# Kernel optimization log

Hardware: AMD Instinct MI355X
Metric: run time of the kernel (lower is better)

Reference implementation:

```python
import jax, jax.numpy as jnp
import numpy as np

OUT_F = 8192
IN_F = 8192
RANK = 32
N_TOK = 128


def _pack_ternary(w_q):
    """Pack int8 ternary {-1,0,+1} [out,in] -> uint8 [out,in//4], LSB-first 2-bit codes."""
    enc = (w_q.astype(np.int32) + 1).astype(np.uint8).reshape(w_q.shape[0], -1, 4)
    packed = enc[:, :, 0] | (enc[:, :, 1] << 2) | (enc[:, :, 2] << 4) | (enc[:, :, 3] << 6)
    return packed


def setup_inputs() -> dict:
    key = jax.random.key(0)
    kx, kw, ks, ka, kb, kbias = jax.random.split(key, 6)
    x = jax.random.normal(kx, (N_TOK, IN_F), dtype=jnp.float32)
    # ternary weights in {-1,0,+1}
    w_q = np.asarray(jax.random.randint(kw, (OUT_F, IN_F), -1, 2, dtype=jnp.int32), dtype=np.int8)
    weight_packed = jnp.asarray(_pack_ternary(w_q), dtype=jnp.uint8)
    scale = jax.random.uniform(ks, (OUT_F,), dtype=jnp.float32, minval=0.01, maxval=0.05)
    lora_A = jax.random.normal(ka, (OUT_F, RANK), dtype=jnp.float32) * 0.02
    lora_B = jax.random.normal(kb, (RANK, IN_F), dtype=jnp.float32) * 0.02
    bias = jax.random.normal(kbias, (OUT_F,), dtype=jnp.float32) * 0.01
    return {"x": x, "weight_packed": weight_packed, "scale": scale,
            "lora_A": lora_A, "lora_B": lora_B, "bias": bias, "in_features": IN_F}


def _unpack_ternary(packed, in_features, dtype):
    # packed: uint8 [out, in//4]; LSB-first 2-bit codes, code-1 -> {-1,0,+1}
    p = packed.astype(jnp.int32)
    vals = jnp.stack([p & 3, (p >> 2) & 3, (p >> 4) & 3, (p >> 6) & 3], axis=-1)
    vals = vals.reshape(packed.shape[0], -1)[:, :in_features] - 1
    return vals.astype(dtype)


def reference(x, weight_packed, scale, lora_A, lora_B, bias, in_features):
    W = _unpack_ternary(weight_packed, in_features, x.dtype)  # [out, in]
    out = (x @ W.T) * scale[None, :]                          # [n, out]
    out = out + (x @ lora_B.T) @ lora_A.T                     # low-rank LoRA path
    out = out + bias
    return out
```

## Files before the change

### kernel.cpp

```cpp
#include <hip/hip_runtime.h>
#include <hip/hip_bf16.h>
#include <stdint.h>

typedef float f32x4 __attribute__((ext_vector_type(4)));
typedef __bf16 bf16x8 __attribute__((ext_vector_type(8)));
typedef unsigned short ushort8 __attribute__((ext_vector_type(8)));

#define N_TOK 128
#define OUT_F 8192
#define IN_F  8192
#define RANK  32

#define KSPLIT 16
#define KB    (IN_F / KSPLIT)
#define BK    64
#define NSTEP (KB / BK)
#define LKC   4

#define XB_OFF 0
#define TB_OFF ((size_t)N_TOK * IN_F * 2)
#define PO_OFF (TB_OFF + (size_t)LKC * N_TOK * RANK * 4)

__device__ __forceinline__ unsigned short bf16r(float f) {
    uint32_t u = __float_as_uint(f);
    return (unsigned short)((u + 0x7FFFu + ((u >> 16) & 1u)) >> 16);
}

__global__ __launch_bounds__(256) void cvt_x(const float* __restrict__ x,
                                             unsigned short* __restrict__ xb) {
    size_t i = ((size_t)blockIdx.x * 256 + threadIdx.x) * 8;
    float4 a = *(const float4*)(x + i);
    float4 b = *(const float4*)(x + i + 4);
    ushort8 o;
    o[0] = bf16r(a.x); o[1] = bf16r(a.y); o[2] = bf16r(a.z); o[3] = bf16r(a.w);
    o[4] = bf16r(b.x); o[5] = bf16r(b.y); o[6] = bf16r(b.z); o[7] = bf16r(b.w);
    *(ushort8*)(xb + i) = o;
}

__global__ __launch_bounds__(256) void lora_t(const float* __restrict__ x,
                                              const float* __restrict__ lb,
                                              float* __restrict__ tB) {
    __shared__ float ts[256][33];
    __shared__ float ps[8][32];
    const int m = blockIdx.x >> 2, kc = blockIdx.x & 3;
    const int tid = threadIdx.x;
    const int c0 = kc * 2048 + tid * 8;
    float4 xv0 = *(const float4*)(x + (size_t)m * IN_F + c0);
    float4 xv1 = *(const float4*)(x + (size_t)m * IN_F + c0 + 4);
#pragma unroll
    for (int r = 0; r < RANK; ++r) {
        const float4* bp = (const float4*)(lb + (size_t)r * IN_F + c0);
        float4 b0 = bp[0], b1 = bp[1];
        float s = xv0.x * b0.x + xv0.y * b0.y + xv0.z * b0.z + xv0.w * b0.w +
                  xv1.x * b1.x + xv1.y * b1.y + xv1.z * b1.z + xv1.w * b1.w;
        ts[tid][r] = s;
    }
    __syncthreads();
    {
        int g = tid >> 5, r = tid & 31;
        float s = 0.f;
        for (int j = 0; j < 32; ++j) s += ts[g * 32 + j][r];
        ps[g][r] = s;
    }
    __syncthreads();
    if (tid < 32) {
        float s = 0.f;
#pragma unroll
        for (int g = 0; g < 8; ++g) s += ps[g][tid];
        tB[(kc * N_TOK + m) * RANK + tid] = s;
    }
}

__device__ __forceinline__ void decode16(uint32_t p, uint32_t d[8]) {
    const uint32_t HI = 0x403F00BFu;
    const uint32_t LO = 0x00800080u;
#pragma unroll
    for (int j = 0; j < 8; ++j) {
        uint32_t c0 = (p >> (4 * j)) & 3u;
        uint32_t c1 = (p >> (4 * j + 2)) & 3u;
        uint32_t t = c0 | (c1 << 16);
        uint32_t sel = (t | (t << 8)) + 0x04000400u;
        d[j] = __builtin_amdgcn_perm(HI, LO, sel);
    }
}

__device__ __forceinline__ int swz(int row, int col) { return col ^ ((row & 7) << 3); }

__global__ __launch_bounds__(256) void ternary_gemm(const unsigned short* __restrict__ xb,
                                                    const int* __restrict__ wp,
                                                    float* __restrict__ pO) {
    __shared__ unsigned short xs[128][64];
    __shared__ unsigned short ww[128][64];
    const int tid = threadIdx.x;
    const int nb = blockIdx.x >> 4;
    const int ks = blockIdx.x & 15;
    const int n0 = nb * 128;
    const int k0 = ks * KB;
    const int lane = tid & 63;
    const int wid = tid >> 6;
    const int wr = wid >> 1, wc = wid & 1;

    const int srow = tid >> 2;
    const int xcol = (tid & 3) * 16;
    const unsigned short* xg0 = xb + (size_t)srow * IN_F + k0 + xcol;
    const unsigned short* xg1 = xg0 + (size_t)64 * IN_F;
    const int pcol = (tid & 3) * 4;
    const int* pg0 = wp + (size_t)(n0 + srow) * (IN_F / 4) + (k0 >> 2) + pcol;
    const int* pg1 = pg0 + (size_t)64 * (IN_F / 4);

    f32x4 acc[4][4];
#pragma unroll
    for (int i = 0; i < 4; ++i)
#pragma unroll
        for (int j = 0; j < 4; ++j) acc[i][j] = (f32x4){0.f, 0.f, 0.f, 0.f};

    const int arow = lane & 15;
    const int kgrp = (lane >> 4) * 8;

    const int wc0 = swz(srow, xcol), wc1 = swz(srow, xcol + 8);

    uint4 cx0a = *(const uint4*)(xg0);
    uint4 cx0b = *(const uint4*)(xg0 + 8);
    uint4 cx1a = *(const uint4*)(xg1);
    uint4 cx1b = *(const uint4*)(xg1 + 8);
    int4 cp0 = *(const int4*)(pg0);
    int4 cp1 = *(const int4*)(pg1);

    for (int s = 0; s < NSTEP; ++s) {
        uint4 nx0a, nx0b, nx1a, nx1b;
        int4 np0, np1;
        if (s + 1 < NSTEP) {
            const unsigned short* a0 = xg0 + (s + 1) * BK;
            const unsigned short* a1 = xg1 + (s + 1) * BK;
            nx0a = *(const uint4*)(a0);
            nx0b = *(const uint4*)(a0 + 8);
            nx1a = *(const uint4*)(a1);
            nx1b = *(const uint4*)(a1 + 8);
            np0 = *(const int4*)(pg0 + (s + 1) * (BK / 4));
            np1 = *(const int4*)(pg1 + (s + 1) * (BK / 4));
        }
        uint32_t p0 = (uint32_t)cp0.x | ((uint32_t)cp0.y << 8) |
                      ((uint32_t)cp0.z << 16) | ((uint32_t)cp0.w << 24);
        uint32_t p1 = (uint32_t)cp1.x | ((uint32_t)cp1.y << 8) |
                      ((uint32_t)cp1.z << 16) | ((uint32_t)cp1.w << 24);
        uint32_t d0[8], d1[8];
        decode16(p0, d0);
        decode16(p1, d1);
        __syncthreads();
        *(uint4*)&xs[srow][wc0] = cx0a;
        *(uint4*)&xs[srow][wc1] = cx0b;
        *(uint4*)&xs[srow + 64][wc0] = cx1a;
        *(uint4*)&xs[srow + 64][wc1] = cx1b;
        *(uint4*)&ww[srow][wc0] = make_uint4(d0[0], d0[1], d0[2], d0[3]);
        *(uint4*)&ww[srow][wc1] = make_uint4(d0[4], d0[5], d0[6], d0[7]);
        *(uint4*)&ww[srow + 64][wc0] = make_uint4(d1[0], d1[1], d1[2], d1[3]);
        *(uint4*)&ww[srow + 64][wc1] = make_uint4(d1[4], d1[5], d1[6], d1[7]);
        __syncthreads();
#pragma unroll
        for (int kk = 0; kk < 2; ++kk) {
            const int kcol = kk * 32 + kgrp;
            bf16x8 af[4], bfr[4];
#pragma unroll
            for (int ar = 0; ar < 4; ++ar) {
                int row = wr * 64 + ar * 16 + arow;
                af[ar] = *(const bf16x8*)&xs[row][swz(row, kcol)];
            }
#pragma unroll
            for (int br = 0; br < 4; ++br) {
                int row = wc * 64 + br * 16 + arow;
                bfr[br] = *(const bf16x8*)&ww[row][swz(row, kcol)];
            }
#pragma unroll
            for (int ar = 0; ar < 4; ++ar)
#pragma unroll
                for (int br = 0; br < 4; ++br)
                    acc[ar][br] = __builtin_amdgcn_mfma_f32_16x16x32_bf16(
                        af[ar], bfr[br], acc[ar][br], 0, 0, 0);
        }
        if (s + 1 < NSTEP) {
            cx0a = nx0a; cx0b = nx0b; cx1a = nx1a; cx1b = nx1b;
            cp0 = np0; cp1 = np1;
        }
    }

    float* po = pO + ((size_t)ks << 20);
    const int mrow = (lane >> 4) * 4;
#pragma unroll
    for (int ar = 0; ar < 4; ++ar) {
#pragma unroll
        for (int br = 0; br < 4; ++br) {
            int m = wr * 64 + ar * 16 + mrow;
            int n = n0 + wc * 64 + br * 16 + arow;
            float* pp = po + (size_t)m * OUT_F + n;
#pragma unroll
            for (int j = 0; j < 4; ++j) pp[(size_t)j * OUT_F] = acc[ar][br][j];
        }
    }
}

__global__ __launch_bounds__(256) void reduce_out(const float* __restrict__ pO,
                                                  const float* __restrict__ tB,
                                                  const float* __restrict__ scale,
                                                  const float* __restrict__ lora_A,
                                                  const float* __restrict__ bias,
                                                  float* __restrict__ out) {
    __shared__ float ts[8][RANK];
    int nb = blockIdx.x & 31, mg = blockIdx.x >> 5;
    int tid = threadIdx.x;
    int m0 = mg * 8;
    {
        int i = tid >> 5, r = tid & 31;
        float s = 0.f;
#pragma unroll
        for (int c = 0; c < LKC; ++c) s += tB[(c * N_TOK + m0 + i) * RANK + r];
        ts[i][r] = s;
    }
    __syncthreads();
    int n = nb * 256 + tid;
    float sc = scale[n], bs = bias[n];
    float4 a4[8];
    const float4* ap = (const float4*)(lora_A + (size_t)n * RANK);
#pragma unroll
    for (int q = 0; q < 8; ++q) a4[q] = ap[q];
#pragma unroll
    for (int i = 0; i < 8; ++i) {
        int m = m0 + i;
        const float* pp = pO + (size_t)m * OUT_F + n;
        float s = 0.f;
#pragma unroll
        for (int c = 0; c < KSPLIT; ++c) s += pp[(size_t)c << 20];
        float l = 0.f;
#pragma unroll
        for (int q = 0; q < 8; ++q) {
            float4 tv = *(const float4*)&ts[i][q * 4];
            l = fmaf(tv.x, a4[q].x, l);
            l = fmaf(tv.y, a4[q].y, l);
            l = fmaf(tv.z, a4[q].z, l);
            l = fmaf(tv.w, a4[q].w, l);
        }
        out[(size_t)m * OUT_F + n] = fmaf(s, sc, l + bs);
    }
}

extern "C" void kernel_launch(void* const* d_in, const int* in_sizes, int n_in,
                              void* d_out, int out_size, void* d_ws, size_t ws_size,
                              hipStream_t stream) {
    const float* x      = (const float*)d_in[0];
    const int*   wp     = (const int*)d_in[1];
    const float* scale  = (const float*)d_in[2];
    const float* lora_A = (const float*)d_in[3];
    const float* lora_B = (const float*)d_in[4];
    const float* bias   = (const float*)d_in[5];
    float* out = (float*)d_out;

    char* ws = (char*)d_ws;
    unsigned short* xb = (unsigned short*)(ws + XB_OFF);
    float* tB = (float*)(ws + TB_OFF);
    float* pO = (float*)(ws + PO_OFF);

    cvt_x<<<(N_TOK * IN_F) / (256 * 8), 256, 0, stream>>>(x, xb);
    lora_t<<<N_TOK * LKC, 256, 0, stream>>>(x, lora_B, tB);
    ternary_gemm<<<(OUT_F / 128) * KSPLIT, 256, 0, stream>>>(xb, wp, pO);
    reduce_out<<<(OUT_F / 256) * (N_TOK / 8), 256, 0, stream>>>(pO, tB, scale, lora_A, bias, out);
}
```

Before: 61.53 us.

## Store split-K partials as bf16 and deepen weight prefetch in ternary GEMM

The GEMM now writes its 16 split-K partial sums as bf16 instead of fp32, which halves the workspace traffic to and from the reduction kernel. The reduce kernel reads two bf16 values per 32-bit load and handles two output columns per thread, with a new grid shape. The GEMM main loop is also restructured: weight tiles are prefetched two steps ahead into alternating registers, and decode is moved after the barrier so it overlaps the MFMAs. The cost is lost precision in the partial sums, since rounding each partial to bf16 adds error before accumulation.

```diff
diff --git a/kernel.cpp b/kernel.cpp
--- a/kernel.cpp
+++ b/kernel.cpp
@@ -15,6 +15,7 @@
 #define KB    (IN_F / KSPLIT)
 #define BK    64
 #define NSTEP (KB / BK)
+#define WSTRIDE 16
 #define LKC   4
 
 #define XB_OFF 0
@@ -71,7 +72,9 @@
     }
 }
 
-__device__ __forceinline__ void decode16(uint32_t p, uint32_t d[8]) {
+__device__ __forceinline__ void decodeW(int4 v, uint32_t d[8]) {
+    uint32_t p = (uint32_t)v.x | ((uint32_t)v.y << 8) |
+                 ((uint32_t)v.z << 16) | ((uint32_t)v.w << 24);
     const uint32_t HI = 0x403F00BFu;
     const uint32_t LO = 0x00800080u;
 #pragma unroll
@@ -88,7 +91,7 @@
 
 __global__ __launch_bounds__(256) void ternary_gemm(const unsigned short* __restrict__ xb,
                                                     const int* __restrict__ wp,
-                                                    float* __restrict__ pO) {
+                                                    unsigned short* __restrict__ pO) {
     __shared__ unsigned short xs[128][64];
     __shared__ unsigned short ww[128][64];
     const int tid = threadIdx.x;
@@ -116,46 +119,58 @@
 
     const int arow = lane & 15;
     const int kgrp = (lane >> 4) * 8;
-
     const int wc0 = swz(srow, xcol), wc1 = swz(srow, xcol + 8);
 
-    uint4 cx0a = *(const uint4*)(xg0);
-    uint4 cx0b = *(const uint4*)(xg0 + 8);
-    uint4 cx1a = *(const uint4*)(xg1);
-    uint4 cx1b = *(const uint4*)(xg1 + 8);
-    int4 cp0 = *(const int4*)(pg0);
-    int4 cp1 = *(const int4*)(pg1);
-
+    uint4 xw0a = *(const uint4*)(xg0);
+    uint4 xw0b = *(const uint4*)(xg0 + 8);
+    uint4 xw1a = *(const uint4*)(xg1);
+    uint4 xw1b = *(const uint4*)(xg1 + 8);
+    uint32_t d0[8], d1[8];
+    int4 w0A, w1A, w0B, w1B;
+    {
+        int4 t0 = *(const int4*)(pg0);
+        int4 t1 = *(const int4*)(pg1);
+        w0A = *(const int4*)(pg0 + WSTRIDE);
+        w1A = *(const int4*)(pg1 + WSTRIDE);
+        decodeW(t0, d0);
+        decodeW(t1, d1);
+    }
+
+#pragma unroll
     for (int s = 0; s < NSTEP; ++s) {
-        uint4 nx0a, nx0b, nx1a, nx1b;
-        int4 np0, np1;
-        if (s + 1 < NSTEP) {
-            const unsigned short* a0 = xg0 + (s + 1) * BK;
-            const unsigned short* a1 = xg1 + (s + 1) * BK;
-            nx0a = *(const uint4*)(a0);
-            nx0b = *(const uint4*)(a0 + 8);
-            nx1a = *(const uint4*)(a1);
-            nx1b = *(const uint4*)(a1 + 8);
-            np0 = *(const int4*)(pg0 + (s + 1) * (BK / 4));
-            np1 = *(const int4*)(pg1 + (s + 1) * (BK / 4));
-        }
-        uint32_t p0 = (uint32_t)cp0.x | ((uint32_t)cp0.y << 8) |
-                      ((uint32_t)cp0.z << 16) | ((uint32_t)cp0.w << 24);
-        uint32_t p1 = (uint32_t)cp1.x | ((uint32_t)cp1.y << 8) |
-                      ((uint32_t)cp1.z << 16) | ((uint32_t)cp1.w << 24);
-        uint32_t d0[8], d1[8];
-        decode16(p0, d0);
-        decode16(p1, d1);
         __syncthreads();
-        *(uint4*)&xs[srow][wc0] = cx0a;
-        *(uint4*)&xs[srow][wc1] = cx0b;
-        *(uint4*)&xs[srow + 64][wc0] = cx1a;
-        *(uint4*)&xs[srow + 64][wc1] = cx1b;
+        *(uint4*)&xs[srow][wc0] = xw0a;
+        *(uint4*)&xs[srow][wc1] = xw0b;
+        *(uint4*)&xs[srow + 64][wc0] = xw1a;
+        *(uint4*)&xs[srow + 64][wc1] = xw1b;
         *(uint4*)&ww[srow][wc0] = make_uint4(d0[0], d0[1], d0[2], d0[3]);
         *(uint4*)&ww[srow][wc1] = make_uint4(d0[4], d0[5], d0[6], d0[7]);
         *(uint4*)&ww[srow + 64][wc0] = make_uint4(d1[0], d1[1], d1[2], d1[3]);
         *(uint4*)&ww[srow + 64][wc1] = make_uint4(d1[4], d1[5], d1[6], d1[7]);
+        if (s + 1 < NSTEP) {
+            const unsigned short* a0 = xg0 + (s + 1) * BK;
+            const unsigned short* a1 = xg1 + (s + 1) * BK;
+            xw0a = *(const uint4*)(a0);
+            xw0b = *(const uint4*)(a0 + 8);
+            xw1a = *(const uint4*)(a1);
+            xw1b = *(const uint4*)(a1 + 8);
+        }
+        if ((s & 1) == 0) {
+            if (s + 2 < NSTEP) {
+                w0B = *(const int4*)(pg0 + (s + 2) * WSTRIDE);
+                w1B = *(const int4*)(pg1 + (s + 2) * WSTRIDE);
+            }
+        } else {
+            if (s + 2 < NSTEP) {
+                w0A = *(const int4*)(pg0 + (s + 2) * WSTRIDE);
+                w1A = *(const int4*)(pg1 + (s + 2) * WSTRIDE);
+            }
+        }
         __syncthreads();
+        if (s + 1 < NSTEP) {
+            if ((s & 1) == 0) { decodeW(w0A, d0); decodeW(w1A, d1); }
+            else              { decodeW(w0B, d0); decodeW(w1B, d1); }
+        }
 #pragma unroll
         for (int kk = 0; kk < 2; ++kk) {
             const int kcol = kk * 32 + kgrp;
@@ -177,13 +192,9 @@
                     acc[ar][br] = __builtin_amdgcn_mfma_f32_16x16x32_bf16(
                         af[ar], bfr[br], acc[ar][br], 0, 0, 0);
         }
-        if (s + 1 < NSTEP) {
-            cx0a = nx0a; cx0b = nx0b; cx1a = nx1a; cx1b = nx1b;
-            cp0 = np0; cp1 = np1;
-        }
-    }
-
-    float* po = pO + ((size_t)ks << 20);
+    }
+
+    unsigned short* po = pO + ((size_t)ks << 20);
     const int mrow = (lane >> 4) * 4;
 #pragma unroll
     for (int ar = 0; ar < 4; ++ar) {
@@ -191,24 +202,24 @@
         for (int br = 0; br < 4; ++br) {
             int m = wr * 64 + ar * 16 + mrow;
             int n = n0 + wc * 64 + br * 16 + arow;
-            float* pp = po + (size_t)m * OUT_F + n;
-#pragma unroll
-            for (int j = 0; j < 4; ++j) pp[(size_t)j * OUT_F] = acc[ar][br][j];
-        }
-    }
-}
-
-__global__ __launch_bounds__(256) void reduce_out(const float* __restrict__ pO,
+            unsigned short* pp = po + (size_t)m * OUT_F + n;
+#pragma unroll
+            for (int j = 0; j < 4; ++j) pp[(size_t)j * OUT_F] = bf16r(acc[ar][br][j]);
+        }
+    }
+}
+
+__global__ __launch_bounds__(256) void reduce_out(const unsigned short* __restrict__ pO,
                                                   const float* __restrict__ tB,
                                                   const float* __restrict__ scale,
                                                   const float* __restrict__ lora_A,
                                                   const float* __restrict__ bias,
                                                   float* __restrict__ out) {
-    __shared__ float ts[8][RANK];
-    int nb = blockIdx.x & 31, mg = blockIdx.x >> 5;
+    __shared__ float ts[4][RANK];
+    int nb = blockIdx.x & 15, mg = blockIdx.x >> 4;
     int tid = threadIdx.x;
-    int m0 = mg * 8;
-    {
+    int m0 = mg * 4;
+    if (tid < 128) {
         int i = tid >> 5, r = tid & 31;
         float s = 0.f;
 #pragma unroll
@@ -216,29 +227,36 @@
         ts[i][r] = s;
     }
     __syncthreads();
-    int n = nb * 256 + tid;
-    float sc = scale[n], bs = bias[n];
-    float4 a4[8];
-    const float4* ap = (const float4*)(lora_A + (size_t)n * RANK);
-#pragma unroll
-    for (int q = 0; q < 8; ++q) a4[q] = ap[q];
-#pragma unroll
-    for (int i = 0; i < 8; ++i) {
+    int n = nb * 512 + tid * 2;
+    float sc0 = scale[n], sc1 = scale[n + 1];
+    float bs0 = bias[n], bs1 = bias[n + 1];
+    float4 a0[8], a1[8];
+    const float4* ap0 = (const float4*)(lora_A + (size_t)n * RANK);
+    const float4* ap1 = (const float4*)(lora_A + (size_t)(n + 1) * RANK);
+#pragma unroll
+    for (int q = 0; q < 8; ++q) { a0[q] = ap0[q]; a1[q] = ap1[q]; }
+#pragma unroll
+    for (int i = 0; i < 4; ++i) {
         int m = m0 + i;
-        const float* pp = pO + (size_t)m * OUT_F + n;
-        float s = 0.f;
-#pragma unroll
-        for (int c = 0; c < KSPLIT; ++c) s += pp[(size_t)c << 20];
-        float l = 0.f;
+        const unsigned short* pp = pO + (size_t)m * OUT_F + n;
+        float s0 = 0.f, s1 = 0.f;
+#pragma unroll
+        for (int c = 0; c < KSPLIT; ++c) {
+            uint32_t u = *(const uint32_t*)(pp + ((size_t)c << 20));
+            s0 += __uint_as_float(u << 16);
+            s1 += __uint_as_float(u & 0xFFFF0000u);
+        }
+        float l0 = 0.f, l1 = 0.f;
 #pragma unroll
         for (int q = 0; q < 8; ++q) {
             float4 tv = *(const float4*)&ts[i][q * 4];
-            l = fmaf(tv.x, a4[q].x, l);
-            l = fmaf(tv.y, a4[q].y, l);
-            l = fmaf(tv.z, a4[q].z, l);
-            l = fmaf(tv.w, a4[q].w, l);
-        }
-        out[(size_t)m * OUT_F + n] = fmaf(s, sc, l + bs);
+            l0 = fmaf(tv.x, a0[q].x, l0); l0 = fmaf(tv.y, a0[q].y, l0);
+            l0 = fmaf(tv.z, a0[q].z, l0); l0 = fmaf(tv.w, a0[q].w, l0);
+            l1 = fmaf(tv.x, a1[q].x, l1); l1 = fmaf(tv.y, a1[q].y, l1);
+            l1 = fmaf(tv.z, a1[q].z, l1); l1 = fmaf(tv.w, a1[q].w, l1);
+        }
+        out[(size_t)m * OUT_F + n]     = fmaf(s0, sc0, l0 + bs0);
+        out[(size_t)m * OUT_F + n + 1] = fmaf(s1, sc1, l1 + bs1);
     }
 }
 
@@ -256,10 +274,10 @@
     char* ws = (char*)d_ws;
     unsigned short* xb = (unsigned short*)(ws + XB_OFF);
     float* tB = (float*)(ws + TB_OFF);
-    float* pO = (float*)(ws + PO_OFF);
+    unsigned short* pO = (unsigned short*)(ws + PO_OFF);
 
     cvt_x<<<(N_TOK * IN_F) / (256 * 8), 256, 0, stream>>>(x, xb);
     lora_t<<<N_TOK * LKC, 256, 0, stream>>>(x, lora_B, tB);
     ternary_gemm<<<(OUT_F / 128) * KSPLIT, 256, 0, stream>>>(xb, wp, pO);
-    reduce_out<<<(OUT_F / 256) * (N_TOK / 8), 256, 0, stream>>>(pO, tB, scale, lora_A, bias, out);
-}
+    reduce_out<<<16 * 32, 256, 0, stream>>>(pO, tB, scale, lora_A, bias, out);
+}
```

Result: faster. 55.06 us (-10.5%).
